# Kernel optimization log

Measured on AMD Instinct MI355X. Metric: run time of the kernel, lower is better.

Reference implementation:

```python
import jax, jax.numpy as jnp
import numpy as np

SR = 22050
FL = 1024      # window_samples
FP = 256       # step_samples
FCEIL = 10000  # formant ceiling (Hz)
MAXF = 4       # max formants
AP_ORDER = 10
R_ORDER = 30
FMIN, FMAX = 50, 500
DK_ITERS = 60  # Durand-Kerner iterations (replaces companion-matrix eig; differentiable)

_w = np.blackman(FL)
WIN = jnp.asarray(_w / np.sqrt(np.sum(_w ** 2)), jnp.float32)  # power-normalized blackman (diffsptk default)


def _frame(x):
    # center-padded framing, frames = T//FP + 1
    pad = FL // 2
    xp = jnp.pad(x, ((0, 0), (pad, pad)))
    n_frames = x.shape[-1] // FP + 1
    idx = jnp.arange(n_frames)[:, None] * FP + jnp.arange(FL)[None, :]
    return xp[:, idx]  # [B, F, FL]


def _levinson(r, order):
    # Levinson-Durbin on autocorrelation r[..., :order+1].
    # Returns (allpole poly coeffs a[..., order+1] with a0=1, reflection coeffs k[..., order]).
    a = jnp.zeros(r.shape[:-1] + (order + 1,), r.dtype).at[..., 0].set(1.0)
    E = r[..., 0]
    ks = []
    for m in range(1, order + 1):
        if m == 1:
            acc = r[..., 1]
        else:
            acc = r[..., m] + jnp.sum(a[..., 1:m] * r[..., m - 1:0:-1], axis=-1)
        k = -acc / (E + 1e-9)
        a_prev = a
        a = a.at[..., m].set(k)
        if m > 1:
            a = a.at[..., 1:m].add(k[..., None] * a_prev[..., m - 1:0:-1])
        E = E * (1.0 - k * k)
        ks.append(k)
    return a, jnp.stack(ks, axis=-1)


def _poly_roots(coeffs):
    # Durand-Kerner simultaneous root iteration, vectorized over frames.
    n = coeffs.shape[-1] - 1
    c = (coeffs / coeffs[..., :1]).astype(jnp.complex64)
    z0 = (0.4 + 0.9j) ** jnp.arange(1, n + 1)
    z = jnp.broadcast_to(z0, c.shape[:-1] + (n,)).astype(jnp.complex64)
    eye = jnp.eye(n, dtype=jnp.complex64)
    def step(z, _):
        p = jnp.zeros_like(z)
        for i in range(n + 1):  # Horner eval of poly at all current root estimates
            p = p * z + c[..., i:i + 1]
        diff = z[..., :, None] - z[..., None, :] + eye
        z = z - p / (jnp.prod(diff, axis=-1) + 1e-12)
        return z, None
    z, _ = jax.lax.scan(step, z, None, length=DK_ITERS)
    return z  # [..., n]


def _root_to_formant(roots):
    # downsampled spectrum covers 0..FCEIL/2, so freq = angle/(2*pi)*FCEIL
    ang = jnp.angle(roots)
    freq = ang / (2.0 * jnp.pi) * FCEIL
    freq = jnp.where(ang > 1e-4, freq, FCEIL * 0.5)  # keep upper-half-plane roots only
    return jnp.sort(freq, axis=-1)[..., :MAXF]  # [B, F, MAXF]


def _pitch(x):
    # autocorrelation pitch tracker
    xf = _frame(x)
    spec = jnp.fft.rfft(xf)
    ac = jnp.fft.irfft(spec * jnp.conj(spec))
    lag_min, lag_max = SR // FMAX, SR // FMIN  # 44..441
    seg = ac[..., lag_min:lag_max + 1]
    peak = jnp.max(seg, axis=-1)
    idx = jnp.argmax(seg, axis=-1)
    nccf = peak / (ac[..., 0] + 1e-9)
    pitch = SR / (lag_min + idx).astype(jnp.float32)
    voicing = (nccf > 0.3).astype(jnp.float32)
    return pitch, voicing, nccf


def _forward(x):
    xf = _frame(x)                 # [B, F, FL]
    xw = xf * WIN
    spec = jnp.fft.rfft(xw)        # [B, F, 513]
    nb = spec.shape[-1]
    ds = int(FCEIL / SR * nb)      # 232 bins -> Nyquist FCEIL/2
    x_ds = spec[..., :ds]
    ac_ds = jnp.fft.irfft(x_ds * jnp.conj(x_ds))   # [B, F, 462]
    ac_us = jnp.fft.irfft(spec * jnp.conj(spec))   # [B, F, 1024]
    ap_env, _ = _levinson(ac_ds, AP_ORDER)
    _, r_coeff_ref = _levinson(ac_us, R_ORDER)
    roots = _poly_roots(ap_env)
    formants = _root_to_formant(roots)
    energy = 10.0 * jnp.log10(jnp.sum(xf * xf, axis=-1) + 1e-10)
    mag = jnp.abs(jnp.fft.rfft(xf))
    freqs = jnp.arange(nb, dtype=jnp.float32) * (SR / FL)
    centroid = jnp.sum(mag * freqs, axis=-1) / (jnp.sum(mag, axis=-1) + 1e-10)
    tilt = ac_ds[..., 1] / (ac_ds[..., 0] + 1e-10)
    pitch, voicing, nccf = _pitch(x)
    pitch = jnp.log(pitch)
    return (formants, energy, centroid, tilt, pitch, voicing, r_coeff_ref, x_ds, nccf)


def setup_inputs() -> dict:
    key = jax.random.key(0)
    x = jax.random.normal(key, (8, 661500), jnp.float32)
    return {"x": x}


def reference(x):
    return _forward(x)
```

## Files before the change

### kernel.cpp

```cpp
#include <hip/hip_runtime.h>
#include <math.h>

#define NSAMP   661500
#define NFRAME  2584
#define NFTOT   20672
#define FPB     6
#define NBLK    3446

#define EN_OFF    82688
#define CEN_OFF   103360
#define TILT_OFF  124032
#define PITCH_OFF 144704
#define VOI_OFF   165376
#define RC_OFF    186048
#define XDS_OFF   806208

__device__ __forceinline__ float waveReduceSum(float v) {
  #pragma unroll
  for (int m = 1; m < 64; m <<= 1) v += __shfl_xor(v, m, 64);
  return v;
}

__device__ __forceinline__ float blockReduceSum(float v, float* s) {
  v = waveReduceSum(v);
  const int w = threadIdx.x >> 6;
  if ((threadIdx.x & 63) == 0) s[w] = v;
  __syncthreads();
  v = s[0] + s[1] + s[2] + s[3];
  __syncthreads();
  return v;
}

__device__ __forceinline__ void fft1024p(float2* X, float2* Y, const float2* tw, int tid) {
  int m = 1;
  #pragma unroll
  for (int s = 0; s < 5; ++s) {
    const int k  = tid & (m - 1);
    const int jm = tid - k;
    const float2 a0 = X[tid];
    const float2 a1 = X[tid + 256];
    const float2 a2 = X[tid + 512];
    const float2 a3 = X[tid + 768];
    const float2 w1 = tw[jm];
    float2 sA, dA, sB, dB;
    sA.x = a0.x + a2.x; sA.y = a0.y + a2.y;
    { const float dx = a0.x - a2.x, dy = a0.y - a2.y;
      dA.x = dx * w1.x + dy * w1.y;
      dA.y = dy * w1.x - dx * w1.y; }
    sB.x = a1.x + a3.x; sB.y = a1.y + a3.y;
    { const float dx = a1.x - a3.x, dy = a1.y - a3.y;
      const float wx = -w1.y, wy = w1.x;
      dB.x = dx * wx + dy * wy;
      dB.y = dy * wx - dx * wy; }
    const float w2x = w1.x * w1.x - w1.y * w1.y;
    const float w2y = 2.0f * w1.x * w1.y;
    const int B = 4 * tid - 3 * k;
    { float2 o;
      o.x = sA.x + sB.x; o.y = sA.y + sB.y;
      Y[B] = o;
      const float dx = sA.x - sB.x, dy = sA.y - sB.y;
      o.x = dx * w2x + dy * w2y;
      o.y = dy * w2x - dx * w2y;
      Y[B + 2 * m] = o; }
    { float2 o;
      o.x = dA.x + dB.x; o.y = dA.y + dB.y;
      Y[B + m] = o;
      const float dx = dA.x - dB.x, dy = dA.y - dB.y;
      o.x = dx * w2x + dy * w2y;
      o.y = dy * w2x - dx * w2y;
      Y[B + 3 * m] = o; }
    __syncthreads();
    float2* tmp = X; X = Y; Y = tmp;
    m <<= 2;
  }
}

template<int ORDER>
__device__ __forceinline__ void levinson_d(const double* r, double* a) {
  double E = r[0];
  a[0] = 1.0;
  #pragma unroll
  for (int m = 1; m <= ORDER; ++m) {
    double acc = r[m];
    #pragma unroll
    for (int i = 1; i < m; ++i) acc += a[i] * r[m - i];
    const double kk = -acc / (E + 1e-9);
    #pragma unroll
    for (int i = 1; i <= (m - 1) / 2; ++i) {
      const double t1 = a[i], t2 = a[m - i];
      a[i]     = t1 + kk * t2;
      a[m - i] = t2 + kk * t1;
    }
    if ((m & 1) == 0) { const double t = a[m >> 1]; a[m >> 1] = t + kk * t; }
    a[m] = kk;
    E *= (1.0 - kk * kk);
  }
}

__device__ __forceinline__ void levinson_f30(const float* r, float* gk) {
  float a[31];
  float E = r[0];
  a[0] = 1.0f;
  #pragma unroll
  for (int m = 1; m <= 30; ++m) {
    float acc = r[m];
    #pragma unroll
    for (int i = 1; i < m; ++i) acc += a[i] * r[m - i];
    const float kk = -acc / (E + 1e-9f);
    #pragma unroll
    for (int i = 1; i <= (m - 1) / 2; ++i) {
      const float t1 = a[i], t2 = a[m - i];
      a[i]     = t1 + kk * t2;
      a[m - i] = t2 + kk * t1;
    }
    if ((m & 1) == 0) { const float t = a[m >> 1]; a[m >> 1] = t + kk * t; }
    a[m] = kk;
    E *= (1.0f - kk * kk);
    if (gk) gk[m - 1] = kk;
  }
}

__global__ void __launch_bounds__(256, 8)
feat_mono6(const float* __restrict__ x, float* __restrict__ out,
           const int xds_pf, const int nccf_off) {
  __shared__ float2 A[1024];
  __shared__ float2 Bb[1024];
  __shared__ float2 tw[256];
  __shared__ float  sred[12];
  __shared__ int    sredi[4];
  __shared__ float  stash[FPB][42];
  __shared__ float  aprt[4][11];

  const int tid   = threadIdx.x;
  const int w     = tid >> 6;
  const int lane  = tid & 63;
  const int fbase = blockIdx.x * FPB;
  const int np    = (fbase + FPB <= NFTOT) ? FPB : (NFTOT - fbase);

  {
    const float th = (float)tid * (6.2831853071795864769f / 1024.0f);
    float sn, cn;
    sincosf(th, &sn, &cn);
    tw[tid] = make_float2(cn, sn);
  }
  float wv[4];
  float wsq = 0.0f;
  #pragma unroll
  for (int q = 0; q < 4; ++q) {
    const int n = tid + q * 256;
    const float th = (float)n * (6.2831853071795864769f / 1023.0f);
    const float wn = 0.42f - 0.5f * cosf(th) + 0.08f * cosf(2.0f * th);
    wv[q] = wn;
    wsq += wn * wn;
  }
  float ctab[11];
  #pragma unroll
  for (int l = 0; l < 11; ++l)
    ctab[l] = cosf((float)(tid * l) * (6.2831853071795864769f / 462.0f));
  const float wgt462 = ((tid == 0 || tid == 231) ? 1.0f : 2.0f) * (1.0f / 462.0f);
  __syncthreads();
  const float invn = 1.0f / sqrtf(blockReduceSum(wsq, sred));

  #pragma unroll 1
  for (int p = 0; p < np; ++p) {
    const int fg = fbase + p;
    const int bb = fg / NFRAME;
    const int fr = fg - bb * NFRAME;
    const float* xb = x + (size_t)bb * NSAMP;

    #pragma unroll
    for (int q = 0; q < 4; ++q) {
      const int n = tid + q * 256;
      const int g = fr * 256 + n - 512;
      const float xv = (g >= 0 && g < NSAMP) ? xb[g] : 0.0f;
      A[n] = make_float2(xv * wv[q] * invn, xv);
    }
    __syncthreads();

    fft1024p(A, Bb, tw, tid);

    float cs0 = 0.0f, cs1 = 0.0f;
    float myPw = 0.0f;
    {
      const int k = tid;
      const float2 Zk = Bb[k];
      const float2 Zn = Bb[(1024 - k) & 1023];
      const float xwr = 0.5f * (Zk.x + Zn.x);
      const float xwi = 0.5f * (Zk.y - Zn.y);
      const float xfr = 0.5f * (Zk.y + Zn.y);
      const float xfi = -0.5f * (Zk.x - Zn.x);
      const float pw = xwr * xwr + xwi * xwi;
      const float pf = xfr * xfr + xfi * xfi;
      const float mg = sqrtf(pf);
      cs0 += mg;
      cs1 += mg * ((float)k * (22050.0f / 1024.0f));
      if (k < 232) {
        myPw = pw;
        if (xds_pf == 232) {
          out[XDS_OFF + (size_t)fg * 232 + k] = xwr;
        } else {
          ((float2*)(out + XDS_OFF))[(size_t)fg * 232 + k] = make_float2(xwr, xwi);
        }
      }
    }
    {
      const int k = tid + 256;
      const float2 Zk = Bb[k];
      const float2 Zn = Bb[1024 - k];
      const float xfr = 0.5f * (Zk.y + Zn.y);
      const float xfi = -0.5f * (Zk.x - Zn.x);
      const float pf = xfr * xfr + xfi * xfi;
      const float mg = sqrtf(pf);
      cs0 += mg;
      cs1 += mg * ((float)k * (22050.0f / 1024.0f));
    }
    if (tid == 0) {
      const int k = 512;
      const float2 Zk = Bb[k];
      const float2 Zn = Bb[512];
      const float xfr = 0.5f * (Zk.y + Zn.y);
      const float xfi = -0.5f * (Zk.x - Zn.x);
      const float pf = xfr * xfr + xfi * xfi;
      const float mg = sqrtf(pf);
      cs0 += mg;
      cs1 += mg * ((float)k * (22050.0f / 1024.0f));
    }

    #pragma unroll
    for (int q = 0; q < 4; ++q) {
      const int k2 = tid + q * 256;
      const int km = (k2 <= 512) ? k2 : (1024 - k2);
      const float2 Zk = Bb[km];
      const float2 Zn = Bb[(1024 - km) & 1023];
      const float xwr = 0.5f * (Zk.x + Zn.x);
      const float xwi = 0.5f * (Zk.y - Zn.y);
      const float xfr = 0.5f * (Zk.y + Zn.y);
      const float xfi = -0.5f * (Zk.x - Zn.x);
      const float pw = xwr * xwr + xwi * xwi;
      const float pf = xfr * xfr + xfi * xfi;
      A[k2] = make_float2(pw * 1024.0f, pf);
    }
    __syncthreads();

    fft1024p(A, Bb, tw, tid);

    float pv = -3.0e38f;
    int   pl = 1 << 30;
    for (int l = 44 + tid; l <= 441; l += 256) {
      const float v = Bb[l].y;
      if (v > pv) { pv = v; pl = l; }
    }
    #pragma unroll
    for (int m = 1; m < 64; m <<= 1) {
      const float ov = __shfl_xor(pv, m, 64);
      const int   ol = __shfl_xor(pl, m, 64);
      if (ov > pv || (ov == pv && ol < pl)) { pv = ov; pl = ol; }
    }
    cs0 = waveReduceSum(cs0);
    cs1 = waveReduceSum(cs1);
    if (lane == 0) { sred[w] = pv; sredi[w] = pl; sred[4 + w] = cs0; sred[8 + w] = cs1; }
    const float pwW = myPw * wgt462;
    #pragma unroll
    for (int l = 0; l < 11; ++l) {
      const float t = waveReduceSum(pwW * ctab[l]);
      if (lane == 0) aprt[w][l] = t;
    }
    __syncthreads();

    if (tid == 0) {
      float bv = sred[0]; int bl = sredi[0];
      #pragma unroll
      for (int q = 1; q < 4; ++q)
        if (sred[q] > bv || (sred[q] == bv && sredi[q] < bl)) { bv = sred[q]; bl = sredi[q]; }
      const float ac0  = Bb[0].y * (1.0f / 1024.0f);
      const float peak = bv * (1.0f / 1024.0f);
      const float nccf = peak / (ac0 + 1e-9f);
      out[PITCH_OFF + fg] = logf(22050.0f / (float)bl);
      out[VOI_OFF + fg]   = (nccf > 0.3f) ? 1.0f : 0.0f;
      out[nccf_off + fg]  = nccf;
      out[EN_OFF + fg]    = 10.0f * log10f(ac0 + 1e-10f);
      const float c0 = sred[4] + sred[5] + sred[6] + sred[7];
      const float c1 = sred[8] + sred[9] + sred[10] + sred[11];
      out[CEN_OFF + fg]   = c1 / (c0 + 1e-10f);
      const float a0 = aprt[0][0] + aprt[1][0] + aprt[2][0] + aprt[3][0];
      const float a1 = aprt[0][1] + aprt[1][1] + aprt[2][1] + aprt[3][1];
      out[TILT_OFF + fg]  = a1 / (a0 + 1e-10f);
    }
    if (tid < 11)
      stash[p][31 + tid] = aprt[0][tid] + aprt[1][tid] + aprt[2][tid] + aprt[3][tid];
    if (tid < 31) stash[p][tid] = Bb[tid].x * (1.0f / 1048576.0f);
  }
  __syncthreads();

  if (w == 0) {
    const int g     = lane / 10;
    const int ri    = lane - g * 10;
    const int gbase = g * 10;
    const int gg    = (g < FPB) ? g : (FPB - 1);
    const bool act  = (g < np);
    const int fg    = fbase + gg;

    levinson_f30(&stash[gg][0],
                 (ri == 0 && act) ? (out + RC_OFF + (size_t)fg * 30) : (float*)nullptr);

    double rds[11], a10[11];
    #pragma unroll
    for (int l = 0; l < 11; ++l) rds[l] = (double)stash[gg][31 + l];
    levinson_d<10>(rds, a10);

    double zr = 0.4, zi = 0.9;
    for (int q = 0; q < ri; ++q) {
      const double nr = zr * 0.4 - zi * 0.9;
      zi = zr * 0.9 + zi * 0.4;
      zr = nr;
    }
    for (int it = 0; it < 60; ++it) {
      double pr = 1.0, pi = 0.0;
      #pragma unroll
      for (int q = 1; q <= 10; ++q) {
        const double nr = pr * zr - pi * zi + a10[q];
        pi = pr * zi + pi * zr;
        pr = nr;
      }
      double dr = 1.0, di = 0.0;
      #pragma unroll
      for (int j = 0; j < 10; ++j) {
        const double ozr = __shfl(zr, gbase + j, 64);
        const double ozi = __shfl(zi, gbase + j, 64);
        const double er = (j == ri) ? 1.0 : (zr - ozr);
        const double ei = (j == ri) ? 0.0 : (zi - ozi);
        const double nr = dr * er - di * ei;
        di = dr * ei + di * er;
        dr = nr;
      }
      dr += 1e-12;
      const double inv = 1.0 / (dr * dr + di * di);
      const double qr = (pr * dr + pi * di) * inv;
      const double qi = (pi * dr - pr * di) * inv;
      zr -= qr;
      zi -= qi;
    }
    const double ang = atan2(zi, zr);
    double freq = (ang > 0.0001) ? (ang / 6.283185307179586476925287 * 10000.0) : 5000.0;
    if (ri >= 10) freq = 1.0e300;

    double f[10];
    #pragma unroll
    for (int j = 0; j < 10; ++j) f[j] = __shfl(freq, gbase + j, 64);
    bool used[10];
    #pragma unroll
    for (int j = 0; j < 10; ++j) used[j] = false;
    float o4[4];
    #pragma unroll
    for (int p2 = 0; p2 < 4; ++p2) {
      double mn = 1.0e300;
      int mj = -1;
      #pragma unroll
      for (int j = 0; j < 10; ++j)
        if (!used[j] && f[j] < mn) { mn = f[j]; mj = j; }
      if (mj >= 0) used[mj] = true;
      o4[p2] = (float)mn;
    }
    if (ri == 0 && act) {
      out[(size_t)fg * 4 + 0] = o4[0];
      out[(size_t)fg * 4 + 1] = o4[1];
      out[(size_t)fg * 4 + 2] = o4[2];
      out[(size_t)fg * 4 + 3] = o4[3];
    }
  }
}

extern "C" void kernel_launch(void* const* d_in, const int* in_sizes, int n_in,
                              void* d_out, int out_size, void* d_ws, size_t ws_size,
                              hipStream_t stream) {
  (void)in_sizes; (void)n_in; (void)d_ws; (void)ws_size;
  const float* x = (const float*)d_in[0];
  float* out = (float*)d_out;
  int xds_pf = 232;
  if (out_size >= XDS_OFF + NFTOT * 464 + NFTOT) xds_pf = 464;
  const int nccf_off = XDS_OFF + NFTOT * xds_pf;
  feat_mono6<<<dim3(NBLK), dim3(256), 0, stream>>>(x, out, xds_pf, nccf_off);
}
```

Measured before the change: 332.4 us.

## Fuse first FFT stage into load, use 8 frames per block, split roots across two waves

Computes the first radix-4 FFT stage in registers straight from the global load and from the power-spectrum build, then writes to shared memory. This removes one shared-memory round trip and one barrier per FFT. Frames per block go from 6 to 8, so the block count divides exactly and the tail handling is dropped. The per-frame Levinson and Durand-Kerner root stage is now spread over two waves (4 frames each) instead of one, which shortens that serial tail but leaves more of each wave's lanes idle.

```diff
diff --git a/kernel.cpp b/kernel.cpp
--- a/kernel.cpp
+++ b/kernel.cpp
@@ -4,8 +4,8 @@
 #define NSAMP   661500
 #define NFRAME  2584
 #define NFTOT   20672
-#define FPB     6
-#define NBLK    3446
+#define FPB     8
+#define NBLK    2584
 
 #define EN_OFF    82688
 #define CEN_OFF   103360
@@ -31,44 +31,48 @@
   return v;
 }
 
-__device__ __forceinline__ void fft1024p(float2* X, float2* Y, const float2* tw, int tid) {
-  int m = 1;
-  #pragma unroll
-  for (int s = 0; s < 5; ++s) {
+__device__ __forceinline__ void fused_bfly(const float2 a0, const float2 a1,
+                                           const float2 a2, const float2 a3,
+                                           const float2 w1, float2* o) {
+  float2 sA, dA, sB, dB;
+  sA.x = a0.x + a2.x; sA.y = a0.y + a2.y;
+  { const float dx = a0.x - a2.x, dy = a0.y - a2.y;
+    dA.x = dx * w1.x + dy * w1.y;
+    dA.y = dy * w1.x - dx * w1.y; }
+  sB.x = a1.x + a3.x; sB.y = a1.y + a3.y;
+  { const float dx = a1.x - a3.x, dy = a1.y - a3.y;
+    const float wx = -w1.y, wy = w1.x;
+    dB.x = dx * wx + dy * wy;
+    dB.y = dy * wx - dx * wy; }
+  const float w2x = w1.x * w1.x - w1.y * w1.y;
+  const float w2y = 2.0f * w1.x * w1.y;
+  o[0].x = sA.x + sB.x; o[0].y = sA.y + sB.y;
+  { const float dx = sA.x - sB.x, dy = sA.y - sB.y;
+    o[2].x = dx * w2x + dy * w2y;
+    o[2].y = dy * w2x - dx * w2y; }
+  o[1].x = dA.x + dB.x; o[1].y = dA.y + dB.y;
+  { const float dx = dA.x - dB.x, dy = dA.y - dB.y;
+    o[3].x = dx * w2x + dy * w2y;
+    o[3].y = dy * w2x - dx * w2y; }
+}
+
+__device__ __forceinline__ void fft4iter(float2* X, float2* Y, const float2* tw, int tid) {
+  int m = 4;
+  #pragma unroll
+  for (int s = 0; s < 4; ++s) {
     const int k  = tid & (m - 1);
     const int jm = tid - k;
     const float2 a0 = X[tid];
     const float2 a1 = X[tid + 256];
     const float2 a2 = X[tid + 512];
     const float2 a3 = X[tid + 768];
-    const float2 w1 = tw[jm];
-    float2 sA, dA, sB, dB;
-    sA.x = a0.x + a2.x; sA.y = a0.y + a2.y;
-    { const float dx = a0.x - a2.x, dy = a0.y - a2.y;
-      dA.x = dx * w1.x + dy * w1.y;
-      dA.y = dy * w1.x - dx * w1.y; }
-    sB.x = a1.x + a3.x; sB.y = a1.y + a3.y;
-    { const float dx = a1.x - a3.x, dy = a1.y - a3.y;
-      const float wx = -w1.y, wy = w1.x;
-      dB.x = dx * wx + dy * wy;
-      dB.y = dy * wx - dx * wy; }
-    const float w2x = w1.x * w1.x - w1.y * w1.y;
-    const float w2y = 2.0f * w1.x * w1.y;
+    float2 o[4];
+    fused_bfly(a0, a1, a2, a3, tw[jm], o);
     const int B = 4 * tid - 3 * k;
-    { float2 o;
-      o.x = sA.x + sB.x; o.y = sA.y + sB.y;
-      Y[B] = o;
-      const float dx = sA.x - sB.x, dy = sA.y - sB.y;
-      o.x = dx * w2x + dy * w2y;
-      o.y = dy * w2x - dx * w2y;
-      Y[B + 2 * m] = o; }
-    { float2 o;
-      o.x = dA.x + dB.x; o.y = dA.y + dB.y;
-      Y[B + m] = o;
-      const float dx = dA.x - dB.x, dy = dA.y - dB.y;
-      o.x = dx * w2x + dy * w2y;
-      o.y = dy * w2x - dx * w2y;
-      Y[B + 3 * m] = o; }
+    Y[B]         = o[0];
+    Y[B + m]     = o[1];
+    Y[B + 2 * m] = o[2];
+    Y[B + 3 * m] = o[3];
     __syncthreads();
     float2* tmp = X; X = Y; Y = tmp;
     m <<= 2;
@@ -121,7 +125,7 @@
 }
 
 __global__ void __launch_bounds__(256, 8)
-feat_mono6(const float* __restrict__ x, float* __restrict__ out,
+feat_mono8(const float* __restrict__ x, float* __restrict__ out,
            const int xds_pf, const int nccf_off) {
   __shared__ float2 A[1024];
   __shared__ float2 Bb[1024];
@@ -135,7 +139,6 @@
   const int w     = tid >> 6;
   const int lane  = tid & 63;
   const int fbase = blockIdx.x * FPB;
-  const int np    = (fbase + FPB <= NFTOT) ? FPB : (NFTOT - fbase);
 
   {
     const float th = (float)tid * (6.2831853071795864769f / 1024.0f);
@@ -160,24 +163,35 @@
   const float wgt462 = ((tid == 0 || tid == 231) ? 1.0f : 2.0f) * (1.0f / 462.0f);
   __syncthreads();
   const float invn = 1.0f / sqrtf(blockReduceSum(wsq, sred));
+  const float2 w1t = tw[tid];
 
   #pragma unroll 1
-  for (int p = 0; p < np; ++p) {
+  for (int p = 0; p < FPB; ++p) {
     const int fg = fbase + p;
     const int bb = fg / NFRAME;
     const int fr = fg - bb * NFRAME;
     const float* xb = x + (size_t)bb * NSAMP;
 
-    #pragma unroll
-    for (int q = 0; q < 4; ++q) {
-      const int n = tid + q * 256;
-      const int g = fr * 256 + n - 512;
-      const float xv = (g >= 0 && g < NSAMP) ? xb[g] : 0.0f;
-      A[n] = make_float2(xv * wv[q] * invn, xv);
+    {
+      float2 z[4];
+      #pragma unroll
+      for (int q = 0; q < 4; ++q) {
+        const int n = tid + q * 256;
+        const int g = fr * 256 + n - 512;
+        const float xv = (g >= 0 && g < NSAMP) ? xb[g] : 0.0f;
+        z[q] = make_float2(xv * wv[q] * invn, xv);
+      }
+      float2 o[4];
+      fused_bfly(z[0], z[1], z[2], z[3], w1t, o);
+      const int B = 4 * tid;
+      Bb[B]     = o[0];
+      Bb[B + 1] = o[1];
+      Bb[B + 2] = o[2];
+      Bb[B + 3] = o[3];
     }
     __syncthreads();
 
-    fft1024p(A, Bb, tw, tid);
+    fft4iter(Bb, A, tw, tid);
 
     float cs0 = 0.0f, cs1 = 0.0f;
     float myPw = 0.0f;
@@ -226,28 +240,38 @@
       cs1 += mg * ((float)k * (22050.0f / 1024.0f));
     }
 
-    #pragma unroll
-    for (int q = 0; q < 4; ++q) {
-      const int k2 = tid + q * 256;
-      const int km = (k2 <= 512) ? k2 : (1024 - k2);
-      const float2 Zk = Bb[km];
-      const float2 Zn = Bb[(1024 - km) & 1023];
-      const float xwr = 0.5f * (Zk.x + Zn.x);
-      const float xwi = 0.5f * (Zk.y - Zn.y);
-      const float xfr = 0.5f * (Zk.y + Zn.y);
-      const float xfi = -0.5f * (Zk.x - Zn.x);
-      const float pw = xwr * xwr + xwi * xwi;
-      const float pf = xfr * xfr + xfi * xfi;
-      A[k2] = make_float2(pw * 1024.0f, pf);
+    {
+      float2 in[4];
+      #pragma unroll
+      for (int q = 0; q < 4; ++q) {
+        const int k2 = tid + q * 256;
+        const int km = (k2 <= 512) ? k2 : (1024 - k2);
+        const float2 Zk = Bb[km];
+        const float2 Zn = Bb[(1024 - km) & 1023];
+        const float xwr = 0.5f * (Zk.x + Zn.x);
+        const float xwi = 0.5f * (Zk.y - Zn.y);
+        const float xfr = 0.5f * (Zk.y + Zn.y);
+        const float xfi = -0.5f * (Zk.x - Zn.x);
+        const float pw = xwr * xwr + xwi * xwi;
+        const float pf = xfr * xfr + xfi * xfi;
+        in[q] = make_float2(pw * 1024.0f, pf);
+      }
+      float2 o[4];
+      fused_bfly(in[0], in[1], in[2], in[3], w1t, o);
+      const int B = 4 * tid;
+      A[B]     = o[0];
+      A[B + 1] = o[1];
+      A[B + 2] = o[2];
+      A[B + 3] = o[3];
     }
     __syncthreads();
 
-    fft1024p(A, Bb, tw, tid);
+    fft4iter(A, Bb, tw, tid);
 
     float pv = -3.0e38f;
     int   pl = 1 << 30;
     for (int l = 44 + tid; l <= 441; l += 256) {
-      const float v = Bb[l].y;
+      const float v = A[l].y;
       if (v > pv) { pv = v; pl = l; }
     }
     #pragma unroll
@@ -272,7 +296,7 @@
       #pragma unroll
       for (int q = 1; q < 4; ++q)
         if (sred[q] > bv || (sred[q] == bv && sredi[q] < bl)) { bv = sred[q]; bl = sredi[q]; }
-      const float ac0  = Bb[0].y * (1.0f / 1024.0f);
+      const float ac0  = A[0].y * (1.0f / 1024.0f);
       const float peak = bv * (1.0f / 1024.0f);
       const float nccf = peak / (ac0 + 1e-9f);
       out[PITCH_OFF + fg] = logf(22050.0f / (float)bl);
@@ -288,16 +312,16 @@
     }
     if (tid < 11)
       stash[p][31 + tid] = aprt[0][tid] + aprt[1][tid] + aprt[2][tid] + aprt[3][tid];
-    if (tid < 31) stash[p][tid] = Bb[tid].x * (1.0f / 1048576.0f);
+    if (tid < 31) stash[p][tid] = A[tid].x * (1.0f / 1048576.0f);
   }
   __syncthreads();
 
-  if (w == 0) {
+  if (w < 2) {
     const int g     = lane / 10;
     const int ri    = lane - g * 10;
     const int gbase = g * 10;
-    const int gg    = (g < FPB) ? g : (FPB - 1);
-    const bool act  = (g < np);
+    const bool act  = (g < 4);
+    const int gg    = act ? (w * 4 + g) : 0;
     const int fg    = fbase + gg;
 
     levinson_f30(&stash[gg][0],
@@ -379,5 +403,5 @@
   int xds_pf = 232;
   if (out_size >= XDS_OFF + NFTOT * 464 + NFTOT) xds_pf = 464;
   const int nccf_off = XDS_OFF + NFTOT * xds_pf;
-  feat_mono6<<<dim3(NBLK), dim3(256), 0, stream>>>(x, out, xds_pf, nccf_off);
-}
+  feat_mono8<<<dim3(NBLK), dim3(256), 0, stream>>>(x, out, xds_pf, nccf_off);
+}
```

Result: slower. 397.9 us (+19.7%).

## Split FFT front stage and Levinson/root-finding tail into separate kernels

Applied to the files above, without the earlier changes.

The monolithic kernel is split into a front kernel that does framing, the FFTs and the reductions, and a tail kernel that runs Levinson and Durand-Kerner root finding. The two stages hand off the 42 per-frame autocorrelation values through the workspace buffer. In the old kernel only wave 0 ran the double-precision tail while the other three waves idled. The tail kernel packs 24 frames per block so all four waves are busy. Spectrum outputs now use nontemporal stores. This costs an extra launch and a global round trip of the intermediate values, and the old single kernel is kept as a fallback when no workspace is available.

```diff
diff --git a/kernel.cpp b/kernel.cpp
--- a/kernel.cpp
+++ b/kernel.cpp
@@ -120,15 +120,85 @@
   }
 }
 
+__device__ __forceinline__ void tail_group(const float* st, float* out,
+                                           int frame, int ri, int gbase, bool act) {
+  levinson_f30(st, (ri == 0 && act) ? (out + RC_OFF + (size_t)frame * 30)
+                                    : (float*)nullptr);
+
+  double rds[11], a10[11];
+  #pragma unroll
+  for (int l = 0; l < 11; ++l) rds[l] = (double)st[31 + l];
+  levinson_d<10>(rds, a10);
+
+  double zr = 0.4, zi = 0.9;
+  for (int q = 0; q < ri; ++q) {
+    const double nr = zr * 0.4 - zi * 0.9;
+    zi = zr * 0.9 + zi * 0.4;
+    zr = nr;
+  }
+  for (int it = 0; it < 60; ++it) {
+    double pr = 1.0, pi = 0.0;
+    #pragma unroll
+    for (int q = 1; q <= 10; ++q) {
+      const double nr = pr * zr - pi * zi + a10[q];
+      pi = pr * zi + pi * zr;
+      pr = nr;
+    }
+    double dr = 1.0, di = 0.0;
+    #pragma unroll
+    for (int j = 0; j < 10; ++j) {
+      const double ozr = __shfl(zr, gbase + j, 64);
+      const double ozi = __shfl(zi, gbase + j, 64);
+      const double er = (j == ri) ? 1.0 : (zr - ozr);
+      const double ei = (j == ri) ? 0.0 : (zi - ozi);
+      const double nr = dr * er - di * ei;
+      di = dr * ei + di * er;
+      dr = nr;
+    }
+    dr += 1e-12;
+    const double inv = 1.0 / (dr * dr + di * di);
+    const double qr = (pr * dr + pi * di) * inv;
+    const double qi = (pi * dr - pr * di) * inv;
+    zr -= qr;
+    zi -= qi;
+  }
+  const double ang = atan2(zi, zr);
+  double freq = (ang > 0.0001) ? (ang / 6.283185307179586476925287 * 10000.0) : 5000.0;
+  if (ri >= 10) freq = 1.0e300;
+
+  double f[10];
+  #pragma unroll
+  for (int j = 0; j < 10; ++j) f[j] = __shfl(freq, gbase + j, 64);
+  bool used[10];
+  #pragma unroll
+  for (int j = 0; j < 10; ++j) used[j] = false;
+  float o4[4];
+  #pragma unroll
+  for (int p2 = 0; p2 < 4; ++p2) {
+    double mn = 1.0e300;
+    int mj = -1;
+    #pragma unroll
+    for (int j = 0; j < 10; ++j)
+      if (!used[j] && f[j] < mn) { mn = f[j]; mj = j; }
+    if (mj >= 0) used[mj] = true;
+    o4[p2] = (float)mn;
+  }
+  if (ri == 0 && act) {
+    out[(size_t)frame * 4 + 0] = o4[0];
+    out[(size_t)frame * 4 + 1] = o4[1];
+    out[(size_t)frame * 4 + 2] = o4[2];
+    out[(size_t)frame * 4 + 3] = o4[3];
+  }
+}
+
 __global__ void __launch_bounds__(256, 8)
-feat_mono6(const float* __restrict__ x, float* __restrict__ out,
-           const int xds_pf, const int nccf_off) {
+feat_front(const float* __restrict__ x, float* __restrict__ out,
+           float* __restrict__ ws, const int xds_pf, const int nccf_off) {
   __shared__ float2 A[1024];
   __shared__ float2 Bb[1024];
   __shared__ float2 tw[256];
   __shared__ float  sred[12];
   __shared__ int    sredi[4];
-  __shared__ float  stash[FPB][42];
   __shared__ float  aprt[4][11];
 
   const int tid   = threadIdx.x;
@@ -197,9 +267,11 @@
       if (k < 232) {
         myPw = pw;
         if (xds_pf == 232) {
-          out[XDS_OFF + (size_t)fg * 232 + k] = xwr;
+          __builtin_nontemporal_store(xwr, &out[XDS_OFF + (size_t)fg * 232 + k]);
         } else {
-          ((float2*)(out + XDS_OFF))[(size_t)fg * 232 + k] = make_float2(xwr, xwi);
+          float* dst = out + XDS_OFF + ((size_t)fg * 232 + k) * 2;
+          __builtin_nontemporal_store(xwr, dst);
+          __builtin_nontemporal_store(xwi, dst + 1);
         }
       }
     }
@@ -287,6 +359,199 @@
       out[TILT_OFF + fg]  = a1 / (a0 + 1e-10f);
     }
     if (tid < 11)
+      ws[(size_t)fg * 42 + 31 + tid] =
+          aprt[0][tid] + aprt[1][tid] + aprt[2][tid] + aprt[3][tid];
+    if (tid < 31)
+      ws[(size_t)fg * 42 + tid] = Bb[tid].x * (1.0f / 1048576.0f);
+  }
+}
+
+__global__ void __launch_bounds__(256)
+feat_tail(const float* __restrict__ ws, float* __restrict__ out) {
+  const int tid  = threadIdx.x;
+  const int w    = tid >> 6;
+  const int lane = tid & 63;
+  const int g    = lane / 10;
+  const int ri   = lane - g * 10;
+  const int gbase = g * 10;
+  int frame = blockIdx.x * 24 + w * 6 + ((g < 6) ? g : 5);
+  const bool act = (g < 6) && (frame < NFTOT);
+  if (frame >= NFTOT) frame = NFTOT - 1;
+
+  float st[42];
+  #pragma unroll
+  for (int j = 0; j < 42; ++j) st[j] = ws[(size_t)frame * 42 + j];
+
+  tail_group(st, out, frame, ri, gbase, act);
+}
+
+__global__ void __launch_bounds__(256, 8)
+feat_mono_fb(const float* __restrict__ x, float* __restrict__ out,
+             const int xds_pf, const int nccf_off) {
+  __shared__ float2 A[1024];
+  __shared__ float2 Bb[1024];
+  __shared__ float2 tw[256];
+  __shared__ float  sred[12];
+  __shared__ int    sredi[4];
+  __shared__ float  stash[FPB][42];
+  __shared__ float  aprt[4][11];
+
+  const int tid   = threadIdx.x;
+  const int w     = tid >> 6;
+  const int lane  = tid & 63;
+  const int fbase = blockIdx.x * FPB;
+  const int np    = (fbase + FPB <= NFTOT) ? FPB : (NFTOT - fbase);
+
+  {
+    const float th = (float)tid * (6.2831853071795864769f / 1024.0f);
+    float sn, cn;
+    sincosf(th, &sn, &cn);
+    tw[tid] = make_float2(cn, sn);
+  }
+  float wv[4];
+  float wsq = 0.0f;
+  #pragma unroll
+  for (int q = 0; q < 4; ++q) {
+    const int n = tid + q * 256;
+    const float th = (float)n * (6.2831853071795864769f / 1023.0f);
+    const float wn = 0.42f - 0.5f * cosf(th) + 0.08f * cosf(2.0f * th);
+    wv[q] = wn;
+    wsq += wn * wn;
+  }
+  float ctab[11];
+  #pragma unroll
+  for (int l = 0; l < 11; ++l)
+    ctab[l] = cosf((float)(tid * l) * (6.2831853071795864769f / 462.0f));
+  const float wgt462 = ((tid == 0 || tid == 231) ? 1.0f : 2.0f) * (1.0f / 462.0f);
+  __syncthreads();
+  const float invn = 1.0f / sqrtf(blockReduceSum(wsq, sred));
+
+  #pragma unroll 1
+  for (int p = 0; p < np; ++p) {
+    const int fg = fbase + p;
+    const int bb = fg / NFRAME;
+    const int fr = fg - bb * NFRAME;
+    const float* xb = x + (size_t)bb * NSAMP;
+
+    #pragma unroll
+    for (int q = 0; q < 4; ++q) {
+      const int n = tid + q * 256;
+      const int g = fr * 256 + n - 512;
+      const float xv = (g >= 0 && g < NSAMP) ? xb[g] : 0.0f;
+      A[n] = make_float2(xv * wv[q] * invn, xv);
+    }
+    __syncthreads();
+
+    fft1024p(A, Bb, tw, tid);
+
+    float cs0 = 0.0f, cs1 = 0.0f;
+    float myPw = 0.0f;
+    {
+      const int k = tid;
+      const float2 Zk = Bb[k];
+      const float2 Zn = Bb[(1024 - k) & 1023];
+      const float xwr = 0.5f * (Zk.x + Zn.x);
+      const float xwi = 0.5f * (Zk.y - Zn.y);
+      const float xfr = 0.5f * (Zk.y + Zn.y);
+      const float xfi = -0.5f * (Zk.x - Zn.x);
+      const float pw = xwr * xwr + xwi * xwi;
+      const float pf = xfr * xfr + xfi * xfi;
+      const float mg = sqrtf(pf);
+      cs0 += mg;
+      cs1 += mg * ((float)k * (22050.0f / 1024.0f));
+      if (k < 232) {
+        myPw = pw;
+        if (xds_pf == 232) {
+          out[XDS_OFF + (size_t)fg * 232 + k] = xwr;
+        } else {
+          ((float2*)(out + XDS_OFF))[(size_t)fg * 232 + k] = make_float2(xwr, xwi);
+        }
+      }
+    }
+    {
+      const int k = tid + 256;
+      const float2 Zk = Bb[k];
+      const float2 Zn = Bb[1024 - k];
+      const float xfr = 0.5f * (Zk.y + Zn.y);
+      const float xfi = -0.5f * (Zk.x - Zn.x);
+      const float pf = xfr * xfr + xfi * xfi;
+      const float mg = sqrtf(pf);
+      cs0 += mg;
+      cs1 += mg * ((float)k * (22050.0f / 1024.0f));
+    }
+    if (tid == 0) {
+      const int k = 512;
+      const float2 Zk = Bb[k];
+      const float2 Zn = Bb[512];
+      const float xfr = 0.5f * (Zk.y + Zn.y);
+      const float xfi = -0.5f * (Zk.x - Zn.x);
+      const float pf = xfr * xfr + xfi * xfi;
+      const float mg = sqrtf(pf);
+      cs0 += mg;
+      cs1 += mg * ((float)k * (22050.0f / 1024.0f));
+    }
+
+    #pragma unroll
+    for (int q = 0; q < 4; ++q) {
+      const int k2 = tid + q * 256;
+      const int km = (k2 <= 512) ? k2 : (1024 - k2);
+      const float2 Zk = Bb[km];
+      const float2 Zn = Bb[(1024 - km) & 1023];
+      const float xwr = 0.5f * (Zk.x + Zn.x);
+      const float xwi = 0.5f * (Zk.y - Zn.y);
+      const float xfr = 0.5f * (Zk.y + Zn.y);
+      const float xfi = -0.5f * (Zk.x - Zn.x);
+      const float pw = xwr * xwr + xwi * xwi;
+      const float pf = xfr * xfr + xfi * xfi;
+      A[k2] = make_float2(pw * 1024.0f, pf);
+    }
+    __syncthreads();
+
+    fft1024p(A, Bb, tw, tid);
+
+    float pv = -3.0e38f;
+    int   pl = 1 << 30;
+    for (int l = 44 + tid; l <= 441; l += 256) {
+      const float v = Bb[l].y;
+      if (v > pv) { pv = v; pl = l; }
+    }
+    #pragma unroll
+    for (int m = 1; m < 64; m <<= 1) {
+      const float ov = __shfl_xor(pv, m, 64);
+      const int   ol = __shfl_xor(pl, m, 64);
+      if (ov > pv || (ov == pv && ol < pl)) { pv = ov; pl = ol; }
+    }
+    cs0 = waveReduceSum(cs0);
+    cs1 = waveReduceSum(cs1);
+    if (lane == 0) { sred[w] = pv; sredi[w] = pl; sred[4 + w] = cs0; sred[8 + w] = cs1; }
+    const float pwW = myPw * wgt462;
+    #pragma unroll
+    for (int l = 0; l < 11; ++l) {
+      const float t = waveReduceSum(pwW * ctab[l]);
+      if (lane == 0) aprt[w][l] = t;
+    }
+    __syncthreads();
+
+    if (tid == 0) {
+      float bv = sred[0]; int bl = sredi[0];
+      #pragma unroll
+      for (int q = 1; q < 4; ++q)
+        if (sred[q] > bv || (sred[q] == bv && sredi[q] < bl)) { bv = sred[q]; bl = sredi[q]; }
+      const float ac0  = Bb[0].y * (1.0f / 1024.0f);
+      const float peak = bv * (1.0f / 1024.0f);
+      const float nccf = peak / (ac0 + 1e-9f);
+      out[PITCH_OFF + fg] = logf(22050.0f / (float)bl);
+      out[VOI_OFF + fg]   = (nccf > 0.3f) ? 1.0f : 0.0f;
+      out[nccf_off + fg]  = nccf;
+      out[EN_OFF + fg]    = 10.0f * log10f(ac0 + 1e-10f);
+      const float c0 = sred[4] + sred[5] + sred[6] + sred[7];
+      const float c1 = sred[8] + sred[9] + sred[10] + sred[11];
+      out[CEN_OFF + fg]   = c1 / (c0 + 1e-10f);
+      const float a0 = aprt[0][0] + aprt[1][0] + aprt[2][0] + aprt[3][0];
+      const float a1 = aprt[0][1] + aprt[1][1] + aprt[2][1] + aprt[3][1];
+      out[TILT_OFF + fg]  = a1 / (a0 + 1e-10f);
+    }
+    if (tid < 11)
       stash[p][31 + tid] = aprt[0][tid] + aprt[1][tid] + aprt[2][tid] + aprt[3][tid];
     if (tid < 31) stash[p][tid] = Bb[tid].x * (1.0f / 1048576.0f);
   }
@@ -299,85 +564,26 @@
     const int gg    = (g < FPB) ? g : (FPB - 1);
     const bool act  = (g < np);
     const int fg    = fbase + gg;
-
-    levinson_f30(&stash[gg][0],
-                 (ri == 0 && act) ? (out + RC_OFF + (size_t)fg * 30) : (float*)nullptr);
-
-    double rds[11], a10[11];
-    #pragma unroll
-    for (int l = 0; l < 11; ++l) rds[l] = (double)stash[gg][31 + l];
-    levinson_d<10>(rds, a10);
-
-    double zr = 0.4, zi = 0.9;
-    for (int q = 0; q < ri; ++q) {
-      const double nr = zr * 0.4 - zi * 0.9;
-      zi = zr * 0.9 + zi * 0.4;
-      zr = nr;
-    }
-    for (int it = 0; it < 60; ++it) {
-      double pr = 1.0, pi = 0.0;
-      #pragma unroll
-      for (int q = 1; q <= 10; ++q) {
-        const double nr = pr * zr - pi * zi + a10[q];
-        pi = pr * zi + pi * zr;
-        pr = nr;
-      }
-      double dr = 1.0, di = 0.0;
-      #pragma unroll
-      for (int j = 0; j < 10; ++j) {
-        const double ozr = __shfl(zr, gbase + j, 64);
-        const double ozi = __shfl(zi, gbase + j, 64);
-        const double er = (j == ri) ? 1.0 : (zr - ozr);
-        const double ei = (j == ri) ? 0.0 : (zi - ozi);
-        const double nr = dr * er - di * ei;
-        di = dr * ei + di * er;
-        dr = nr;
-      }
-      dr += 1e-12;
-      const double inv = 1.0 / (dr * dr + di * di);
-      const double qr = (pr * dr + pi * di) * inv;
-      const double qi = (pi * dr - pr * di) * inv;
-      zr -= qr;
-      zi -= qi;
-    }
-    const double ang = atan2(zi, zr);
-    double freq = (ang > 0.0001) ? (ang / 6.283185307179586476925287 * 10000.0) : 5000.0;
-    if (ri >= 10) freq = 1.0e300;
-
-    double f[10];
-    #pragma unroll
-    for (int j = 0; j < 10; ++j) f[j] = __shfl(freq, gbase + j, 64);
-    bool used[10];
-    #pragma unroll
-    for (int j = 0; j < 10; ++j) used[j] = false;
-    float o4[4];
-    #pragma unroll
-    for (int p2 = 0; p2 < 4; ++p2) {
-      double mn = 1.0e300;
-      int mj = -1;
-      #pragma unroll
-      for (int j = 0; j < 10; ++j)
-        if (!used[j] && f[j] < mn) { mn = f[j]; mj = j; }
-      if (mj >= 0) used[mj] = true;
-      o4[p2] = (float)mn;
-    }
-    if (ri == 0 && act) {
-      out[(size_t)fg * 4 + 0] = o4[0];
-      out[(size_t)fg * 4 + 1] = o4[1];
-      out[(size_t)fg * 4 + 2] = o4[2];
-      out[(size_t)fg * 4 + 3] = o4[3];
-    }
+    tail_group(&stash[gg][0], out, fg, ri, gbase, act);
   }
 }
 
 extern "C" void kernel_launch(void* const* d_in, const int* in_sizes, int n_in,
                               void* d_out, int out_size, void* d_ws, size_t ws_size,
                               hipStream_t stream) {
-  (void)in_sizes; (void)n_in; (void)d_ws; (void)ws_size;
+  (void)in_sizes; (void)n_in;
   const float* x = (const float*)d_in[0];
   float* out = (float*)d_out;
   int xds_pf = 232;
   if (out_size >= XDS_OFF + NFTOT * 464 + NFTOT) xds_pf = 464;
   const int nccf_off = XDS_OFF + NFTOT * xds_pf;
-  feat_mono6<<<dim3(NBLK), dim3(256), 0, stream>>>(x, out, xds_pf, nccf_off);
-}
+
+  const size_t need = (size_t)NFTOT * 42 * 4;
+  if (d_ws != nullptr && ws_size >= need) {
+    float* ws = (float*)d_ws;
+    feat_front<<<dim3(NBLK), dim3(256), 0, stream>>>(x, out, ws, xds_pf, nccf_off);
+    feat_tail<<<dim3((NFTOT + 23) / 24), dim3(256), 0, stream>>>(ws, out);
+  } else {
+    feat_mono_fb<<<dim3(NBLK), dim3(256), 0, stream>>>(x, out, xds_pf, nccf_off);
+  }
+}
```

Result: no change. 327.7 us (-1.4%).
